# Kernel optimization log

Measured on AMD Instinct MI355X. Metric: run time of the kernel, lower is better.

Reference implementation:

```python
import jax, jax.numpy as jnp
import numpy as np


def _ste_round(r):
    # straight-through round
    return r + jax.lax.stop_gradient(jnp.round(r) - r)


def quant_sym(x, s, qn, qp):
    # symmetric LSQ-style fake-quant: clamp(round(x/s)) * s
    r = jnp.clip(x / s, qn, qp)
    return _ste_round(r) * s


def quant_asym(x, s, beta, qn, qp):
    # asymmetric fake-quant with learnable zero-point beta
    r = jnp.clip((x - beta) / s, qn, qp)
    return _ste_round(r) * s + beta


def quant_weight_statsq(w, n_bits=8):
    # statsq: per-output-channel scale from weight statistics
    qp = 2 ** (n_bits - 1) - 1          # 127
    qn = -(2 ** (n_bits - 1))           # -128
    s = 2.0 * jnp.mean(jnp.abs(w), axis=1, keepdims=True) / jnp.sqrt(float(qp))
    return quant_sym(w, s, qn, qp)


def setup_inputs() -> dict:
    key = jax.random.key(0)
    ks = jax.random.split(key, 8)
    B, N, C, H = 4, 4096, 1024, 4096
    x = jax.random.normal(ks[0], (B, N, C), dtype=jnp.float32)
    w1 = jax.random.normal(ks[1], (H, C), dtype=jnp.float32) * (1.0 / np.sqrt(C))
    b1 = jax.random.normal(ks[2], (H,), dtype=jnp.float32) * 0.01
    w2 = jax.random.normal(ks[3], (C, H), dtype=jnp.float32) * (1.0 / np.sqrt(H))
    b2 = jax.random.normal(ks[4], (C,), dtype=jnp.float32) * 0.01
    # learnable LSQ activation scales (per input channel), kept positive
    s_a1 = 0.05 + 0.05 * jax.random.uniform(ks[5], (C,), dtype=jnp.float32)
    s_a2 = 0.02 + 0.02 * jax.random.uniform(ks[6], (H,), dtype=jnp.float32)
    beta2 = jnp.zeros((H,), dtype=jnp.float32)
    return {"x": x, "w1": w1, "b1": b1, "w2": w2, "b2": b2,
            "s_a1": s_a1, "s_a2": s_a2, "beta2": beta2}


def reference(x, w1, b1, w2, b2, s_a1, s_a2, beta2):
    # fc1: symmetric 8-bit LSQ on input, statsq 8-bit on weight
    xq = quant_sym(x, s_a1, -128, 127)
    wq1 = quant_weight_statsq(w1)
    h = jnp.einsum('bnc,hc->bnh', xq, wq1) + b1
    h = jax.nn.gelu(h, approximate=False)  # nn.GELU default (exact erf)
    # drop1 = identity in eval
    # fc2: asymmetric 8-bit LSQ on (non-negative-skewed) activations
    hq = quant_asym(h, s_a2, beta2, 0, 255)
    wq2 = quant_weight_statsq(w2)
    out = jnp.einsum('bnh,ch->bnc', hq, wq2) + b2
    # drop2 = identity in eval
    return out
```

## Files before the change

kernel.cpp:

```cpp
#include <hip/hip_runtime.h>
#include <cstdint>
#include <cstddef>

typedef __attribute__((ext_vector_type(8))) short short8;
typedef __attribute__((ext_vector_type(4))) float f32x4;
typedef __attribute__((ext_vector_type(4))) unsigned short ushort4_t;

__device__ __forceinline__ unsigned short f2bf(float f) {
  unsigned u = __float_as_uint(f);
  u += 0x7FFFu + ((u >> 16) & 1u);
  return (unsigned short)(u >> 16);
}

__device__ __forceinline__ void gload_lds16(const void* g, void* lds) {
  __builtin_amdgcn_global_load_lds((const __attribute__((address_space(1))) void*)g,
                                   (__attribute__((address_space(3))) void*)lds,
                                   16, 0, 0);
}

__device__ __forceinline__ float erf_fast(float v) {
  float x = fabsf(v);
  float t = __builtin_amdgcn_rcpf(fmaf(0.3275911f, x, 1.0f));
  float p = fmaf(1.061405429f, t, -1.453152027f);
  p = fmaf(p, t, 1.421413741f);
  p = fmaf(p, t, -0.284496736f);
  p = fmaf(p, t, 0.254829592f);
  p = p * t;
  float e = fmaf(-p, __expf(-x * x), 1.0f);
  unsigned s = __float_as_uint(v) & 0x80000000u;
  return __uint_as_float(__float_as_uint(e) | s);
}

__global__ void quant_x_kernel(const float4* __restrict__ x, const float* __restrict__ s_a1,
                               ushort4_t* __restrict__ xq, int n4, int c4mask) {
  const int stride = gridDim.x * blockDim.x;
  for (int i = blockIdx.x * blockDim.x + threadIdx.x; i < n4; i += stride) {
    float4 v = x[i];
    int c = (i & c4mask) << 2;
    float vv[4] = {v.x, v.y, v.z, v.w};
    ushort4_t o;
#pragma unroll
    for (int j = 0; j < 4; ++j) {
      float s = s_a1[c + j];
      float r = vv[j] / s;
      r = fminf(fmaxf(r, -128.f), 127.f);
      o[j] = f2bf(rintf(r) * s);
    }
    xq[i] = o;
  }
}

__global__ void quant_w_kernel(const float* __restrict__ w, unsigned short* __restrict__ wq,
                               int cols) {
  const int row = blockIdx.x;
  const float* wr = w + (size_t)row * cols;
  float part = 0.f;
  for (int j = threadIdx.x; j < cols; j += blockDim.x) part += fabsf(wr[j]);
#pragma unroll
  for (int o = 32; o > 0; o >>= 1) part += __shfl_down(part, o, 64);
  __shared__ float wsum[4];
  if ((threadIdx.x & 63) == 0) wsum[threadIdx.x >> 6] = part;
  __syncthreads();
  float mean = (wsum[0] + wsum[1] + wsum[2] + wsum[3]) / (float)cols;
  float s = 2.f * mean / sqrtf(127.f);
  unsigned short* wqr = wq + (size_t)row * cols;
  for (int j = threadIdx.x; j < cols; j += blockDim.x) {
    float r = wr[j] / s;
    r = fminf(fmaxf(r, -128.f), 127.f);
    wqr[j] = f2bf(rintf(r) * s);
  }
}

#define BAR() { asm volatile("" ::: "memory"); __builtin_amdgcn_s_barrier(); asm volatile("" ::: "memory"); }
#define SB() __builtin_amdgcn_sched_barrier(0)
#define LGKM(n) { asm volatile("s_waitcnt lgkmcnt(" #n ")" ::: "memory"); SB(); }
#define VMC(n) { asm volatile("s_waitcnt vmcnt(" #n ")" ::: "memory"); SB(); }
#define PRIO1() __builtin_amdgcn_s_setprio(1)
#define PRIO0() __builtin_amdgcn_s_setprio(0)

#define STG(gbase, ldsbuf, h, kt) { \
  _Pragma("unroll") for (int i_ = 0; i_ < 2; ++i_) { \
    const int rb_ = (h) * 128 + (w * 2 + i_) * 8; \
    gload_lds16((gbase) + (size_t)rb_ * K + (size_t)(kt) * 64, (void*)((ldsbuf) + rb_ * 64)); } }

#define LDA_(dst, buf, mh) { \
  _Pragma("unroll") for (int mi_ = 0; mi_ < 4; ++mi_) { \
    dst[mi_][0] = *(const short8*)((buf) + aBase + (mh) * 4096 + mi_ * 1024 + ck0); \
    dst[mi_][1] = *(const short8*)((buf) + aBase + (mh) * 4096 + mi_ * 1024 + ck1); } }

#define LDBX(dst, buf, base) { \
  _Pragma("unroll") for (int ni_ = 0; ni_ < 2; ++ni_) { \
    dst[ni_][0] = *(const short8*)((buf) + (base) + ni_ * 1024 + ck0); \
    dst[ni_][1] = *(const short8*)((buf) + (base) + ni_ * 1024 + ck1); } }

#define MMQ(aR, bR, mh, nh) { \
  _Pragma("unroll") for (int kk_ = 0; kk_ < 2; ++kk_) \
  _Pragma("unroll") for (int mi_ = 0; mi_ < 4; ++mi_) \
  _Pragma("unroll") for (int ni_ = 0; ni_ < 2; ++ni_) \
    acc[(mh) * 4 + mi_][(nh) * 2 + ni_] = __builtin_amdgcn_mfma_f32_16x16x32_bf16( \
        aR[mi_][kk_], bR[ni_][kk_], acc[(mh) * 4 + mi_][(nh) * 2 + ni_], 0, 0, 0); }

template <int EPI>
__global__ __launch_bounds__(512, 2) void gemm_bt_cf(
    const unsigned short* __restrict__ A, const unsigned short* __restrict__ B,
    const float* __restrict__ bias, const float* __restrict__ s2,
    const float* __restrict__ beta, unsigned short* __restrict__ Cq,
    float* __restrict__ Cf, int N, int K)
{
  __shared__ __align__(16) unsigned short As0[256 * 64];
  __shared__ __align__(16) unsigned short As1[256 * 64];
  __shared__ __align__(16) unsigned short Bs0[256 * 64];
  __shared__ __align__(16) unsigned short Bs1[256 * 64];

  const int tid = threadIdx.x;
  const int w = tid >> 6, ll = tid & 63;
  const int wr = w >> 2, wc = w & 3;

  const int nwg = gridDim.x * gridDim.y;
  const int bid = blockIdx.x + gridDim.x * blockIdx.y;
  const int cpx = nwg >> 3;
  const int swz = (bid & 7) * cpx + (bid >> 3);
  const int gy = gridDim.y;
  const int bx = swz / gy, by = swz - bx * gy;
  const long bm = (long)bx * 256;
  const long bn = (long)by * 256;

  const int srow = ll >> 3;
  const int scol = ((ll & 7) ^ srow) << 3;
  const unsigned short* Agl = A + ((size_t)bm + srow) * K + scol;
  const unsigned short* Bgl = B + ((size_t)bn + srow) * K + scol;

  const int lhi = ll >> 4, llo = ll & 15, l7 = ll & 7;
  const int ck0 = ((0 * 4 + lhi) ^ l7) * 8;
  const int ck1 = ((1 * 4 + lhi) ^ l7) * 8;
  const int aBase = (wr * 128 + llo) * 64;
  const int bBase0 = (wc * 32 + llo) * 64;
  const int bBase1 = (128 + wc * 32 + llo) * 64;

  f32x4 acc[8][4] = {};
  short8 a0[4][2], a1[4][2], b0[2][2], b1[2][2];

  const int nkt = K >> 6;

  STG(Bgl, Bs0, 0, 0); STG(Agl, As0, 0, 0); STG(Agl, As0, 1, 0); STG(Bgl, Bs0, 1, 0);
  STG(Bgl, Bs1, 0, 1); STG(Agl, As1, 0, 1); STG(Agl, As1, 1, 1);
  VMC(6);
  BAR();
  LDA_(a0, As0, 0); SB();
  LDBX(b1, Bs0, bBase1); SB();

  for (int t = 0; t < nkt; ++t) {
    unsigned short* Asb = (t & 1) ? As1 : As0;
    unsigned short* Bsb = (t & 1) ? Bs1 : Bs0;
    unsigned short* Asn = (t & 1) ? As0 : As1;
    unsigned short* Bsn = (t & 1) ? Bs0 : Bs1;
    const bool i1 = (t + 1 < nkt), i2 = (t + 2 < nkt);

    BAR();
    LDBX(b0, Bsb, bBase0); SB();
    if (i1) STG(Bgl, Bsn, 1, t + 1);
    LGKM(0);
    PRIO1(); MMQ(a0, b0, 0, 0); PRIO0();

    BAR();
    LDA_(a1, Asb, 1); SB();
    if (i2) STG(Bgl, Bsb, 0, t + 2);
    PRIO1(); MMQ(a0, b1, 0, 1); PRIO0();

    if (i2) { VMC(6); } else { VMC(0); }
    BAR();
    if (i1) { LDA_(a0, Asn, 0); SB(); }
    if (i2) STG(Agl, Asb, 0, t + 2);
    if (i1) { LGKM(8); } else { LGKM(0); }
    PRIO1(); MMQ(a1, b1, 1, 1); PRIO0();

    if (i2) { VMC(4); } else { VMC(0); }
    BAR();
    if (i1) { LDBX(b1, Bsn, bBase1); SB(); }
    if (i2) STG(Agl, Asb, 1, t + 2);
    PRIO1(); MMQ(a1, b0, 1, 0); PRIO0();
  }

  const int lr = lhi;
  const int lc = llo;
#pragma unroll
  for (int NI = 0; NI < 4; ++NI) {
    const long col = bn + wc * 32 + ((NI >= 2) ? 128 : 0) + (NI & 1) * 16 + lc;
    const float bv = bias[col];
    float sv = 1.f, bev = 0.f, inv = 1.f;
    if (EPI == 0) { sv = s2[col]; bev = beta[col]; inv = 1.0f / sv; }
#pragma unroll
    for (int MI = 0; MI < 8; ++MI) {
#pragma unroll
      for (int r = 0; r < 4; ++r) {
        const size_t rowg = (size_t)(bm + wr * 128 + MI * 16 + lr * 4 + r);
        float v = acc[MI][NI][r] + bv;
        if (EPI == 0) {
          float g = 0.5f * v * (1.f + erf_fast(v * 0.70710678118654752f));
          float rr = (g - bev) * inv;
          rr = fminf(fmaxf(rr, 0.f), 255.f);
          Cq[rowg * N + col] = f2bf(fmaf(rintf(rr), sv, bev));
        } else {
          Cf[rowg * N + col] = v;
        }
      }
    }
  }
}

extern "C" void kernel_launch(void* const* d_in, const int* in_sizes, int n_in,
                              void* d_out, int out_size, void* d_ws, size_t ws_size,
                              hipStream_t stream) {
  const float* x     = (const float*)d_in[0];
  const float* w1    = (const float*)d_in[1];
  const float* b1    = (const float*)d_in[2];
  const float* w2    = (const float*)d_in[3];
  const float* b2    = (const float*)d_in[4];
  const float* s_a1  = (const float*)d_in[5];
  const float* s_a2  = (const float*)d_in[6];
  const float* beta2 = (const float*)d_in[7];
  float* out = (float*)d_out;

  const int C = 1024, H = 4096;
  const int M = in_sizes[0] / C;

  unsigned short* xq  = (unsigned short*)d_ws;
  unsigned short* wq1 = xq  + (size_t)M * C;
  unsigned short* wq2 = wq1 + (size_t)H * C;
  unsigned short* hq  = wq2 + (size_t)C * H;

  quant_x_kernel<<<2048, 256, 0, stream>>>((const float4*)x, s_a1, (ushort4_t*)xq,
                                           M * C / 4, C / 4 - 1);
  quant_w_kernel<<<H, 256, 0, stream>>>(w1, wq1, C);
  quant_w_kernel<<<C, 256, 0, stream>>>(w2, wq2, H);

  dim3 g1(M / 256, H / 256);
  gemm_bt_cf<0><<<g1, 512, 0, stream>>>(xq, wq1, b1, s_a2, beta2, hq, nullptr, H, C);
  dim3 g2(M / 256, C / 256);
  gemm_bt_cf<1><<<g2, 512, 0, stream>>>(hq, wq2, b2, nullptr, nullptr, nullptr, out, C, H);
}
```

Baseline: 363.9 us.

## Restructure GEMM main loop into 2x-unrolled whole-tile double buffering with fewer barriers

Replaces the staggered half-tile staging pipeline with a simpler scheme. A full 64-wide K tile is loaded into the alternate LDS buffer while the current one is computed, and the loop is unrolled by two so buffer indices become compile-time constants. Each K tile now uses one barrier instead of four, and LDS addresses come from precomputed pointers into a single shared array. The cost is weaker overlap: a full vmcnt(0) and lgkmcnt(0) wait happens before each barrier, so global-load latency may be exposed.

Result: slower. 456.6 us (+25.5%).

```diff
diff --git a/kernel.cpp b/kernel.cpp
--- a/kernel.cpp
+++ b/kernel.cpp
@@ -73,25 +73,26 @@
 
 #define BAR() { asm volatile("" ::: "memory"); __builtin_amdgcn_s_barrier(); asm volatile("" ::: "memory"); }
 #define SB() __builtin_amdgcn_sched_barrier(0)
-#define LGKM(n) { asm volatile("s_waitcnt lgkmcnt(" #n ")" ::: "memory"); SB(); }
+#define LGKM0() { asm volatile("s_waitcnt lgkmcnt(0)" ::: "memory"); SB(); }
 #define VMC(n) { asm volatile("s_waitcnt vmcnt(" #n ")" ::: "memory"); SB(); }
 #define PRIO1() __builtin_amdgcn_s_setprio(1)
 #define PRIO0() __builtin_amdgcn_s_setprio(0)
 
-#define STG(gbase, ldsbuf, h, kt) { \
-  _Pragma("unroll") for (int i_ = 0; i_ < 2; ++i_) { \
-    const int rb_ = (h) * 128 + (w * 2 + i_) * 8; \
-    gload_lds16((gbase) + (size_t)rb_ * K + (size_t)(kt) * 64, (void*)((ldsbuf) + rb_ * 64)); } }
-
-#define LDA_(dst, buf, mh) { \
+#define LDA(dst, BUF, mh) { \
   _Pragma("unroll") for (int mi_ = 0; mi_ < 4; ++mi_) { \
-    dst[mi_][0] = *(const short8*)((buf) + aBase + (mh) * 4096 + mi_ * 1024 + ck0); \
-    dst[mi_][1] = *(const short8*)((buf) + aBase + (mh) * 4096 + mi_ * 1024 + ck1); } }
-
-#define LDBX(dst, buf, base) { \
+    dst[mi_][0] = *(const short8*)(aP0 + (BUF) * 16384 + (mh) * 4096 + mi_ * 1024); \
+    dst[mi_][1] = *(const short8*)(aP1 + (BUF) * 16384 + (mh) * 4096 + mi_ * 1024); } }
+#define LDB(dst, BUF, nh) { \
   _Pragma("unroll") for (int ni_ = 0; ni_ < 2; ++ni_) { \
-    dst[ni_][0] = *(const short8*)((buf) + (base) + ni_ * 1024 + ck0); \
-    dst[ni_][1] = *(const short8*)((buf) + (base) + ni_ * 1024 + ck1); } }
+    dst[ni_][0] = *(const short8*)(bP0 + (BUF) * 16384 + (nh) * 8192 + ni_ * 1024); \
+    dst[ni_][1] = *(const short8*)(bP1 + (BUF) * 16384 + (nh) * 8192 + ni_ * 1024); } }
+
+#define STGA(BUF, h, px, kadd) { \
+  gload_lds16((px) + (kadd), (void*)(lds + (BUF) * 16384 + (h) * 8192 + w * 1024)); \
+  gload_lds16((px) + (kadd) + rK8, (void*)(lds + (BUF) * 16384 + (h) * 8192 + w * 1024 + 512)); }
+#define STGB(BUF, h, px, kadd) { \
+  gload_lds16((px) + (kadd), (void*)(lds + 32768 + (BUF) * 16384 + (h) * 8192 + w * 1024)); \
+  gload_lds16((px) + (kadd) + rK8, (void*)(lds + 32768 + (BUF) * 16384 + (h) * 8192 + w * 1024 + 512)); }
 
 #define MMQ(aR, bR, mh, nh) { \
   _Pragma("unroll") for (int kk_ = 0; kk_ < 2; ++kk_) \
@@ -101,16 +102,13 @@
         aR[mi_][kk_], bR[ni_][kk_], acc[(mh) * 4 + mi_][(nh) * 2 + ni_], 0, 0, 0); }
 
 template <int EPI>
-__global__ __launch_bounds__(512, 2) void gemm_bt_cf(
+__global__ __launch_bounds__(512, 2) void gemm_bt_wf(
     const unsigned short* __restrict__ A, const unsigned short* __restrict__ B,
     const float* __restrict__ bias, const float* __restrict__ s2,
     const float* __restrict__ beta, unsigned short* __restrict__ Cq,
     float* __restrict__ Cf, int N, int K)
 {
-  __shared__ __align__(16) unsigned short As0[256 * 64];
-  __shared__ __align__(16) unsigned short As1[256 * 64];
-  __shared__ __align__(16) unsigned short Bs0[256 * 64];
-  __shared__ __align__(16) unsigned short Bs1[256 * 64];
+  __shared__ __align__(16) unsigned short lds[65536];
 
   const int tid = threadIdx.x;
   const int w = tid >> 6, ll = tid & 63;
@@ -129,56 +127,61 @@
   const int scol = ((ll & 7) ^ srow) << 3;
   const unsigned short* Agl = A + ((size_t)bm + srow) * K + scol;
   const unsigned short* Bgl = B + ((size_t)bn + srow) * K + scol;
+  const int rK8 = 8 * K;
+  const unsigned short* pA0 = Agl + (size_t)(w * 16) * K;
+  const unsigned short* pA1 = Agl + (size_t)(128 + w * 16) * K;
+  const unsigned short* pB0 = Bgl + (size_t)(w * 16) * K;
+  const unsigned short* pB1 = Bgl + (size_t)(128 + w * 16) * K;
 
   const int lhi = ll >> 4, llo = ll & 15, l7 = ll & 7;
   const int ck0 = ((0 * 4 + lhi) ^ l7) * 8;
   const int ck1 = ((1 * 4 + lhi) ^ l7) * 8;
-  const int aBase = (wr * 128 + llo) * 64;
-  const int bBase0 = (wc * 32 + llo) * 64;
-  const int bBase1 = (128 + wc * 32 + llo) * 64;
+  const unsigned short* aP0 = lds + (wr * 128 + llo) * 64 + ck0;
+  const unsigned short* aP1 = lds + (wr * 128 + llo) * 64 + ck1;
+  const unsigned short* bP0 = lds + 32768 + (wc * 32 + llo) * 64 + ck0;
+  const unsigned short* bP1 = lds + 32768 + (wc * 32 + llo) * 64 + ck1;
 
   f32x4 acc[8][4] = {};
   short8 a0[4][2], a1[4][2], b0[2][2], b1[2][2];
 
   const int nkt = K >> 6;
 
-  STG(Bgl, Bs0, 0, 0); STG(Agl, As0, 0, 0); STG(Agl, As0, 1, 0); STG(Bgl, Bs0, 1, 0);
-  STG(Bgl, Bs1, 0, 1); STG(Agl, As1, 0, 1); STG(Agl, As1, 1, 1);
-  VMC(6);
+  STGA(0, 0, pA0, 0); STGA(0, 1, pA1, 0); STGB(0, 0, pB0, 0); STGB(0, 1, pB1, 0);
+  STGA(1, 0, pA0, 64); STGA(1, 1, pA1, 64); STGB(1, 0, pB0, 64); STGB(1, 1, pB1, 64);
+  pA0 += 128; pA1 += 128; pB0 += 128; pB1 += 128;
+  VMC(8);
   BAR();
-  LDA_(a0, As0, 0); SB();
-  LDBX(b1, Bs0, bBase1); SB();
-
-  for (int t = 0; t < nkt; ++t) {
-    unsigned short* Asb = (t & 1) ? As1 : As0;
-    unsigned short* Bsb = (t & 1) ? Bs1 : Bs0;
-    unsigned short* Asn = (t & 1) ? As0 : As1;
-    unsigned short* Bsn = (t & 1) ? Bs0 : Bs1;
-    const bool i1 = (t + 1 < nkt), i2 = (t + 2 < nkt);
-
-    BAR();
-    LDBX(b0, Bsb, bBase0); SB();
-    if (i1) STG(Bgl, Bsn, 1, t + 1);
-    LGKM(0);
+  LDA(a0, 0, 0); SB();
+
+  for (int t = 0; t < nkt; t += 2) {
+    const bool i2e = (t + 2 < nkt);
+    const bool i1o = i2e, i2o = (t + 3 < nkt);
+
+    LDB(b0, 0, 0); LGKM0(); LDB(b1, 0, 1); SB();
     PRIO1(); MMQ(a0, b0, 0, 0); PRIO0();
-
-    BAR();
-    LDA_(a1, Asb, 1); SB();
-    if (i2) STG(Bgl, Bsb, 0, t + 2);
+    LGKM0(); LDA(a1, 0, 1); SB();
     PRIO1(); MMQ(a0, b1, 0, 1); PRIO0();
-
-    if (i2) { VMC(6); } else { VMC(0); }
-    BAR();
-    if (i1) { LDA_(a0, Asn, 0); SB(); }
-    if (i2) STG(Agl, Asb, 0, t + 2);
-    if (i1) { LGKM(8); } else { LGKM(0); }
+    LGKM0(); VMC(0); BAR();
+    LDA(a0, 1, 0); SB();
+    if (i2e) { STGA(0, 0, pA0, 0); STGA(0, 1, pA1, 0); } SB();
     PRIO1(); MMQ(a1, b1, 1, 1); PRIO0();
-
-    if (i2) { VMC(4); } else { VMC(0); }
-    BAR();
-    if (i1) { LDBX(b1, Bsn, bBase1); SB(); }
-    if (i2) STG(Agl, Asb, 1, t + 2);
+    LGKM0();
+    if (i2e) { STGB(0, 0, pB0, 0); STGB(0, 1, pB1, 0); } SB();
     PRIO1(); MMQ(a1, b0, 1, 0); PRIO0();
+
+    LDB(b0, 1, 0); LGKM0(); LDB(b1, 1, 1); SB();
+    PRIO1(); MMQ(a0, b0, 0, 0); PRIO0();
+    LGKM0(); LDA(a1, 1, 1); SB();
+    PRIO1(); MMQ(a0, b1, 0, 1); PRIO0();
+    LGKM0(); VMC(0); BAR();
+    if (i1o) { LDA(a0, 0, 0); SB(); }
+    if (i2o) { STGA(1, 0, pA0, 64); STGA(1, 1, pA1, 64); } SB();
+    PRIO1(); MMQ(a1, b1, 1, 1); PRIO0();
+    LGKM0();
+    if (i2o) { STGB(1, 0, pB0, 64); STGB(1, 1, pB1, 64); } SB();
+    PRIO1(); MMQ(a1, b0, 1, 0); PRIO0();
+
+    pA0 += 128; pA1 += 128; pB0 += 128; pB1 += 128;
   }
 
   const int lr = lhi;
@@ -235,7 +238,7 @@
   quant_w_kernel<<<C, 256, 0, stream>>>(w2, wq2, H);
 
   dim3 g1(M / 256, H / 256);
-  gemm_bt_cf<0><<<g1, 512, 0, stream>>>(xq, wq1, b1, s_a2, beta2, hq, nullptr, H, C);
+  gemm_bt_wf<0><<<g1, 512, 0, stream>>>(xq, wq1, b1, s_a2, beta2, hq, nullptr, H, C);
   dim3 g2(M / 256, C / 256);
-  gemm_bt_cf<1><<<g2, 512, 0, stream>>>(hq, wq2, b2, nullptr, nullptr, nullptr, out, C, H);
-}
+  gemm_bt_wf<1><<<g2, 512, 0, stream>>>(hq, wq2, b2, nullptr, nullptr, nullptr, out, C, H);
+}
```
